# Performance work log

Measured on AMD Instinct MI355X. Metric: run time of the kernel, lower is better.

Reference implementation:

```python
import jax, jax.numpy as jnp
import numpy as np

EPS = 1e-4
B, D, DOUT = 8192, 4096, 4096


def setup_inputs() -> dict:
    key = jax.random.key(0)
    k1, k2, k3 = jax.random.split(key, 3)
    x = jax.random.normal(k1, (B, D), dtype=jnp.float32)
    # Linear layer params (torch nn.Linear: y = x @ W.T + b)
    W = jax.random.normal(k2, (DOUT, D), dtype=jnp.float32) * (1.0 / np.sqrt(D))
    b = jax.random.normal(k3, (DOUT,), dtype=jnp.float32) * 0.01
    return {"x": x, "W": W, "b": b}


def reference(x, W, b):
    # hess = sum_b x[b] outer x[b] + eps*I  == X^T X + eps*I (a GEMM, not a
    # materialized [B,D,D] broadcast like the torch source)
    d = x.shape[1]
    hess = jnp.einsum('bi,bj->ij', x, x) + EPS * jnp.eye(d, dtype=x.dtype)
    out = x @ W.T + b  # wrapped nn.Linear
    return out, hess
```

## Files before the change

kernel.cpp:

```cpp
#include <hip/hip_runtime.h>
#include <hip/hip_bf16.h>

#define BDIM 8192
#define DDIM 4096
#define DOUTD 4096

typedef __attribute__((ext_vector_type(8))) short short8;
typedef __attribute__((ext_vector_type(16))) float floatx16;

__device__ inline unsigned short f32_to_bf16_rne(float f) {
    unsigned int u = __float_as_uint(f);
    unsigned int lsb = (u >> 16) & 1u;
    u += 0x7fffu + lsb;
    return (unsigned short)(u >> 16);
}

__device__ inline void gload_lds16(const void* g, void* lds) {
    __builtin_amdgcn_global_load_lds(
        (const __attribute__((address_space(1))) void*)g,
        (__attribute__((address_space(3))) void*)lds,
        16, 0, 0);
}

__global__ __launch_bounds__(256)
void convert_transpose_x(const float* __restrict__ x,
                         unsigned short* __restrict__ xb,
                         unsigned short* __restrict__ xT) {
    __shared__ __align__(16) unsigned short tile[64][72];
    const int t = threadIdx.x;
    const int tb = blockIdx.x * 64;
    const int td = blockIdx.y * 64;
#pragma unroll
    for (int p = 0; p < 4; ++p) {
        int c = t + p * 256;
        int row  = c >> 4;
        int col4 = (c & 15) << 2;
        float4 v = *(const float4*)&x[(size_t)(tb + row) * DDIM + td + col4];
        ushort4 o;
        o.x = f32_to_bf16_rne(v.x);
        o.y = f32_to_bf16_rne(v.y);
        o.z = f32_to_bf16_rne(v.z);
        o.w = f32_to_bf16_rne(v.w);
        *(ushort4*)&xb[(size_t)(tb + row) * DDIM + td + col4] = o;
        tile[col4 + 0][row] = o.x;
        tile[col4 + 1][row] = o.y;
        tile[col4 + 2][row] = o.z;
        tile[col4 + 3][row] = o.w;
    }
    __syncthreads();
#pragma unroll
    for (int p = 0; p < 4; ++p) {
        int c = t + p * 256;
        int drow = c >> 4;
        int b4   = (c & 15) << 2;
        ushort4 o = *(const ushort4*)&tile[drow][b4];
        *(ushort4*)&xT[(size_t)(td + drow) * BDIM + tb + b4] = o;
    }
}

__global__ __launch_bounds__(256)
void convert_w_kernel(const float* __restrict__ W, unsigned short* __restrict__ Wb) {
    size_t i = ((size_t)blockIdx.x * 256 + threadIdx.x) * 4;
    float4 v = *(const float4*)&W[i];
    ushort4 o;
    o.x = f32_to_bf16_rne(v.x);
    o.y = f32_to_bf16_rne(v.y);
    o.z = f32_to_bf16_rne(v.z);
    o.w = f32_to_bf16_rne(v.w);
    *(ushort4*)&Wb[i] = o;
}

#define CFENCE() asm volatile("" ::: "memory")
#define BAR() do { CFENCE(); __builtin_amdgcn_s_barrier(); CFENCE(); } while (0)
#define MFMA_BF16 __builtin_amdgcn_mfma_f32_32x32x16_bf16

template <bool HESS>
__global__ __launch_bounds__(512, 2)
void gemm256(const unsigned short* __restrict__ A,
             const unsigned short* __restrict__ B,
             const float* __restrict__ bias,
             float* __restrict__ C,
             int M, int N, int K) {
    __shared__ __align__(16) unsigned short As[32768];
    __shared__ __align__(16) unsigned short Bs[32768];

    const int t    = threadIdx.x;
    const int lane = t & 63;
    const int w    = t >> 6;
    const int lm   = lane & 31;
    const int hi   = lane >> 5;
    const int key2 = (lm >> 2) & 3;
    const int wm   = w >> 2;
    const int wn   = w & 3;
    const size_t bm = (size_t)blockIdx.y * 256;
    const size_t bn = (size_t)blockIdx.x * 256;
    const int NT = K >> 6;

    const int kh_w = w >> 2;
    const int wq   = w & 3;
    const int rsub = lane >> 2;
    const int csrc = (lane & 3) ^ ((lane >> 4) & 3);
    const unsigned short* gA0 = A + (bm + wq * 32 + rsub) * (size_t)K + kh_w * 32 + csrc * 8;
    const unsigned short* gB0 = B + (bn + wq * 32 + rsub) * (size_t)K + kh_w * 32 + csrc * 8;
    char* ldsA = (char*)As + kh_w * 16384 + wq * 2048;
    char* ldsB = (char*)Bs + kh_w * 16384 + wq * 2048;
    const size_t rowK16 = (size_t)16 * K;
    const size_t halfK  = (size_t)128 * K;

#define STAGE_A(tj, h, buf) do {                                   \
        const size_t _ko = (size_t)(tj) * 64 + (size_t)(h) * halfK;\
        char* _d = ldsA + (buf) * 32768 + (h) * 8192;              \
        gload_lds16(gA0 + _ko, _d);                                \
        gload_lds16(gA0 + _ko + rowK16, _d + 1024);                \
    } while (0)
#define STAGE_B(tj, h, buf) do {                                   \
        const size_t _ko = (size_t)(tj) * 64 + (size_t)(h) * halfK;\
        char* _d = ldsB + (buf) * 32768 + (h) * 8192;              \
        gload_lds16(gB0 + _ko, _d);                                \
        gload_lds16(gB0 + _ko + rowK16, _d + 1024);                \
    } while (0)

    const int AROWb = (wm * 128 + lm) * 32;
    const int BROWb = (wn * 32 + lm) * 32;
    int pofs[4];
#pragma unroll
    for (int s = 0; s < 4; ++s)
        pofs[s] = (s >> 1) * 8192 + ((((s & 1) * 2 + hi) ^ key2) * 8);

    floatx16 acc[4][2];
#pragma unroll
    for (int i = 0; i < 4; ++i)
#pragma unroll
        for (int j = 0; j < 2; ++j)
#pragma unroll
            for (int g = 0; g < 16; ++g)
                acc[i][j][g] = 0.f;

    short8 af0[2][4], af1[2][4], bf[4];

    STAGE_B(0, 0, 0);
    STAGE_A(0, 0, 0);
    STAGE_A(0, 1, 0);
    STAGE_B(0, 1, 0);
    STAGE_B(1, 0, 1);
    STAGE_A(1, 0, 1);
    STAGE_A(1, 1, 1);
    asm volatile("s_waitcnt vmcnt(6)" ::: "memory");
    BAR();

    for (int j = 0; j < NT; ++j) {
        const int cur = j & 1;
        const int ab  = cur * 16384;

#pragma unroll
        for (int mi = 0; mi < 2; ++mi)
#pragma unroll
            for (int s = 0; s < 4; ++s)
                af0[mi][s] = *(const short8*)&As[ab + AROWb + mi * 1024 + pofs[s]];
#pragma unroll
        for (int s = 0; s < 4; ++s)
            bf[s] = *(const short8*)&Bs[ab + BROWb + pofs[s]];
        if (j + 1 < NT) STAGE_B(j + 1, 1, cur ^ 1);
        BAR();
        __builtin_amdgcn_s_setprio(1);
#pragma unroll
        for (int s = 0; s < 4; ++s) {
            acc[0][0] = MFMA_BF16(af0[0][s], bf[s], acc[0][0], 0, 0, 0);
            acc[1][0] = MFMA_BF16(af0[1][s], bf[s], acc[1][0], 0, 0, 0);
        }
        __builtin_amdgcn_s_setprio(0);
        asm volatile("s_waitcnt lgkmcnt(0)" ::: "memory");
        BAR();

#pragma unroll
        for (int mi = 0; mi < 2; ++mi)
#pragma unroll
            for (int s = 0; s < 4; ++s)
                af1[mi][s] = *(const short8*)&As[ab + AROWb + 2048 + mi * 1024 + pofs[s]];
        if (j + 2 < NT) STAGE_B(j + 2, 0, cur);
        BAR();
        __builtin_amdgcn_s_setprio(1);
#pragma unroll
        for (int s = 0; s < 4; ++s) {
            acc[2][0] = MFMA_BF16(af1[0][s], bf[s], acc[2][0], 0, 0, 0);
            acc[3][0] = MFMA_BF16(af1[1][s], bf[s], acc[3][0], 0, 0, 0);
        }
        __builtin_amdgcn_s_setprio(0);
        asm volatile("s_waitcnt lgkmcnt(0)" ::: "memory");
        BAR();

#pragma unroll
        for (int s = 0; s < 4; ++s)
            bf[s] = *(const short8*)&Bs[ab + BROWb + 4096 + pofs[s]];
        if (j + 2 < NT) STAGE_A(j + 2, 0, cur);
        BAR();
        __builtin_amdgcn_s_setprio(1);
#pragma unroll
        for (int s = 0; s < 4; ++s) {
            acc[2][1] = MFMA_BF16(af1[0][s], bf[s], acc[2][1], 0, 0, 0);
            acc[3][1] = MFMA_BF16(af1[1][s], bf[s], acc[3][1], 0, 0, 0);
        }
        __builtin_amdgcn_s_setprio(0);
        asm volatile("s_waitcnt lgkmcnt(0)" ::: "memory");
        BAR();

        if (j + 2 < NT) STAGE_A(j + 2, 1, cur);
        BAR();
        __builtin_amdgcn_s_setprio(1);
#pragma unroll
        for (int s = 0; s < 4; ++s) {
            acc[0][1] = MFMA_BF16(af0[0][s], bf[s], acc[0][1], 0, 0, 0);
            acc[1][1] = MFMA_BF16(af0[1][s], bf[s], acc[1][1], 0, 0, 0);
        }
        __builtin_amdgcn_s_setprio(0);
        if (j < NT - 2)       asm volatile("s_waitcnt vmcnt(6)" ::: "memory");
        else if (j == NT - 2) asm volatile("s_waitcnt vmcnt(0)" ::: "memory");
        BAR();
    }
#undef STAGE_A
#undef STAGE_B

    float bv[2];
#pragma unroll
    for (int n2 = 0; n2 < 2; ++n2)
        bv[n2] = HESS ? 0.f : bias[bn + n2 * 128 + wn * 32 + lm];
#pragma unroll
    for (int m4 = 0; m4 < 4; ++m4) {
        const size_t mbase = bm + wm * 128 + (m4 >> 1) * 64 + (m4 & 1) * 32 + 4 * hi;
#pragma unroll
        for (int n2 = 0; n2 < 2; ++n2) {
            const size_t n = bn + n2 * 128 + wn * 32 + lm;
#pragma unroll
            for (int reg = 0; reg < 16; ++reg) {
                const size_t m = mbase + (reg & 3) + 8 * (reg >> 2);
                float v = acc[m4][n2][reg] + bv[n2];
                if (HESS && m == n) v += 1e-4f;
                C[m * N + n] = v;
            }
        }
    }
}

extern "C" void kernel_launch(void* const* d_in, const int* in_sizes, int n_in,
                              void* d_out, int out_size, void* d_ws, size_t ws_size,
                              hipStream_t stream) {
    const float* x = (const float*)d_in[0];
    const float* W = (const float*)d_in[1];
    const float* b = (const float*)d_in[2];

    float* out  = (float*)d_out;
    float* hess = out + (size_t)BDIM * DOUTD;

    unsigned short* xb = (unsigned short*)d_ws;
    unsigned short* xT = xb + (size_t)BDIM * DDIM;
    unsigned short* Wb = xT + (size_t)BDIM * DDIM;

    convert_transpose_x<<<dim3(BDIM / 64, DDIM / 64), 256, 0, stream>>>(x, xb, xT);
    convert_w_kernel<<<((size_t)DOUTD * DDIM) / 1024, 256, 0, stream>>>(W, Wb);

    gemm256<false><<<dim3(DOUTD / 256, BDIM / 256), 512, 0, stream>>>(
        xb, Wb, b, out, BDIM, DOUTD, DDIM);
    gemm256<true><<<dim3(DDIM / 256, DDIM / 256), 512, 0, stream>>>(
        xT, xT, nullptr, hess, DDIM, DDIM, BDIM);
}
```

Measured before the change: 858.7 us.

## Restructure GEMM main loop into k-slice phases with register double-buffered fragments

```diff
diff --git a/kernel.cpp b/kernel.cpp
--- a/kernel.cpp
+++ b/kernel.cpp
@@ -96,36 +96,37 @@
     const size_t bn = (size_t)blockIdx.x * 256;
     const int NT = K >> 6;
 
-    const int kh_w = w >> 2;
-    const int wq   = w & 3;
     const int rsub = lane >> 2;
     const int csrc = (lane & 3) ^ ((lane >> 4) & 3);
-    const unsigned short* gA0 = A + (bm + wq * 32 + rsub) * (size_t)K + kh_w * 32 + csrc * 8;
-    const unsigned short* gB0 = B + (bn + wq * 32 + rsub) * (size_t)K + kh_w * 32 + csrc * 8;
-    char* ldsA = (char*)As + kh_w * 16384 + wq * 2048;
-    char* ldsB = (char*)Bs + kh_w * 16384 + wq * 2048;
+    const unsigned short* gA0 = A + (bm + w * 32 + rsub) * (size_t)K + csrc * 8;
+    const unsigned short* gB0 = B + (bn + w * 32 + rsub) * (size_t)K + csrc * 8;
+    char* ldsA = (char*)As + w * 2048;
+    char* ldsB = (char*)Bs + w * 2048;
     const size_t rowK16 = (size_t)16 * K;
-    const size_t halfK  = (size_t)128 * K;
-
-#define STAGE_A(tj, h, buf) do {                                   \
-        const size_t _ko = (size_t)(tj) * 64 + (size_t)(h) * halfK;\
-        char* _d = ldsA + (buf) * 32768 + (h) * 8192;              \
+
+#define STAGE_A(tj, r, buf) do {                                   \
+        const size_t _ko = (size_t)(tj) * 64 + (size_t)(r) * 32;   \
+        char* _d = ldsA + (buf) * 32768 + (r) * 16384;             \
         gload_lds16(gA0 + _ko, _d);                                \
         gload_lds16(gA0 + _ko + rowK16, _d + 1024);                \
     } while (0)
-#define STAGE_B(tj, h, buf) do {                                   \
-        const size_t _ko = (size_t)(tj) * 64 + (size_t)(h) * halfK;\
-        char* _d = ldsB + (buf) * 32768 + (h) * 8192;              \
+#define STAGE_B(tj, r, buf) do {                                   \
+        const size_t _ko = (size_t)(tj) * 64 + (size_t)(r) * 32;   \
+        char* _d = ldsB + (buf) * 32768 + (r) * 16384;             \
         gload_lds16(gB0 + _ko, _d);                                \
         gload_lds16(gB0 + _ko + rowK16, _d + 1024);                \
     } while (0)
 
-    const int AROWb = (wm * 128 + lm) * 32;
-    const int BROWb = (wn * 32 + lm) * 32;
-    int pofs[4];
+    const int arow0 = (wm * 128 +  0 + lm) * 32;
+    const int arow1 = (wm * 128 + 32 + lm) * 32;
+    const int arow2 = (wm * 128 + 64 + lm) * 32;
+    const int arow3 = (wm * 128 + 96 + lm) * 32;
+    const int brow0 = (  0 + wn * 32 + lm) * 32;
+    const int brow1 = (128 + wn * 32 + lm) * 32;
+    int pos[4];
 #pragma unroll
     for (int s = 0; s < 4; ++s)
-        pofs[s] = (s >> 1) * 8192 + ((((s & 1) * 2 + hi) ^ key2) * 8);
+        pos[s] = (s >> 1) * 8192 + ((((s & 1) * 2 + hi) ^ key2) * 8);
 
     floatx16 acc[4][2];
 #pragma unroll
@@ -136,89 +137,83 @@
             for (int g = 0; g < 16; ++g)
                 acc[i][j][g] = 0.f;
 
-    short8 af0[2][4], af1[2][4], bf[4];
-
-    STAGE_B(0, 0, 0);
-    STAGE_A(0, 0, 0);
-    STAGE_A(0, 1, 0);
-    STAGE_B(0, 1, 0);
-    STAGE_B(1, 0, 1);
-    STAGE_A(1, 0, 1);
-    STAGE_A(1, 1, 1);
+    short8 af[2][4], bf[2][2];
+
+#define READS(tt, bufofs, set) do {                                 \
+        const int _o = (bufofs) + pos[tt];                          \
+        af[set][0] = *(const short8*)&As[_o + arow0];               \
+        af[set][1] = *(const short8*)&As[_o + arow1];               \
+        af[set][2] = *(const short8*)&As[_o + arow2];               \
+        af[set][3] = *(const short8*)&As[_o + arow3];               \
+        bf[set][0] = *(const short8*)&Bs[_o + brow0];               \
+        bf[set][1] = *(const short8*)&Bs[_o + brow1];               \
+    } while (0)
+
+#define MM(set) do {                                                        \
+        acc[0][0] = MFMA_BF16(af[set][0], bf[set][0], acc[0][0], 0, 0, 0);  \
+        acc[1][0] = MFMA_BF16(af[set][1], bf[set][0], acc[1][0], 0, 0, 0);  \
+        acc[2][0] = MFMA_BF16(af[set][2], bf[set][0], acc[2][0], 0, 0, 0);  \
+        acc[3][0] = MFMA_BF16(af[set][3], bf[set][0], acc[3][0], 0, 0, 0);  \
+        acc[0][1] = MFMA_BF16(af[set][0], bf[set][1], acc[0][1], 0, 0, 0);  \
+        acc[1][1] = MFMA_BF16(af[set][1], bf[set][1], acc[1][1], 0, 0, 0);  \
+        acc[2][1] = MFMA_BF16(af[set][2], bf[set][1], acc[2][1], 0, 0, 0);  \
+        acc[3][1] = MFMA_BF16(af[set][3], bf[set][1], acc[3][1], 0, 0, 0);  \
+    } while (0)
+
+    STAGE_B(0, 0, 0); STAGE_A(0, 0, 0); STAGE_B(0, 1, 0); STAGE_A(0, 1, 0);
+    STAGE_B(1, 0, 1); STAGE_A(1, 0, 1); STAGE_B(1, 1, 1);
     asm volatile("s_waitcnt vmcnt(6)" ::: "memory");
     BAR();
+    READS(0, 0, 0);
 
     for (int j = 0; j < NT; ++j) {
-        const int cur = j & 1;
-        const int ab  = cur * 16384;
-
-#pragma unroll
-        for (int mi = 0; mi < 2; ++mi)
-#pragma unroll
-            for (int s = 0; s < 4; ++s)
-                af0[mi][s] = *(const short8*)&As[ab + AROWb + mi * 1024 + pofs[s]];
-#pragma unroll
-        for (int s = 0; s < 4; ++s)
-            bf[s] = *(const short8*)&Bs[ab + BROWb + pofs[s]];
-        if (j + 1 < NT) STAGE_B(j + 1, 1, cur ^ 1);
-        BAR();
-        __builtin_amdgcn_s_setprio(1);
-#pragma unroll
-        for (int s = 0; s < 4; ++s) {
-            acc[0][0] = MFMA_BF16(af0[0][s], bf[s], acc[0][0], 0, 0, 0);
-            acc[1][0] = MFMA_BF16(af0[1][s], bf[s], acc[1][0], 0, 0, 0);
-        }
-        __builtin_amdgcn_s_setprio(0);
-        asm volatile("s_waitcnt lgkmcnt(0)" ::: "memory");
-        BAR();
-
-#pragma unroll
-        for (int mi = 0; mi < 2; ++mi)
-#pragma unroll
-            for (int s = 0; s < 4; ++s)
-                af1[mi][s] = *(const short8*)&As[ab + AROWb + 2048 + mi * 1024 + pofs[s]];
-        if (j + 2 < NT) STAGE_B(j + 2, 0, cur);
-        BAR();
-        __builtin_amdgcn_s_setprio(1);
-#pragma unroll
-        for (int s = 0; s < 4; ++s) {
-            acc[2][0] = MFMA_BF16(af1[0][s], bf[s], acc[2][0], 0, 0, 0);
-            acc[3][0] = MFMA_BF16(af1[1][s], bf[s], acc[3][0], 0, 0, 0);
-        }
-        __builtin_amdgcn_s_setprio(0);
-        asm volatile("s_waitcnt lgkmcnt(0)" ::: "memory");
-        BAR();
-
-#pragma unroll
-        for (int s = 0; s < 4; ++s)
-            bf[s] = *(const short8*)&Bs[ab + BROWb + 4096 + pofs[s]];
-        if (j + 2 < NT) STAGE_A(j + 2, 0, cur);
-        BAR();
-        __builtin_amdgcn_s_setprio(1);
-#pragma unroll
-        for (int s = 0; s < 4; ++s) {
-            acc[2][1] = MFMA_BF16(af1[0][s], bf[s], acc[2][1], 0, 0, 0);
-            acc[3][1] = MFMA_BF16(af1[1][s], bf[s], acc[3][1], 0, 0, 0);
-        }
-        __builtin_amdgcn_s_setprio(0);
-        asm volatile("s_waitcnt lgkmcnt(0)" ::: "memory");
-        BAR();
-
-        if (j + 2 < NT) STAGE_A(j + 2, 1, cur);
-        BAR();
-        __builtin_amdgcn_s_setprio(1);
-#pragma unroll
-        for (int s = 0; s < 4; ++s) {
-            acc[0][1] = MFMA_BF16(af0[0][s], bf[s], acc[0][1], 0, 0, 0);
-            acc[1][1] = MFMA_BF16(af0[1][s], bf[s], acc[1][1], 0, 0, 0);
-        }
-        __builtin_amdgcn_s_setprio(0);
-        if (j < NT - 2)       asm volatile("s_waitcnt vmcnt(6)" ::: "memory");
-        else if (j == NT - 2) asm volatile("s_waitcnt vmcnt(0)" ::: "memory");
-        BAR();
-    }
+        const int b   = j & 1;
+        const int ab  = b * 16384;
+        const int ab2 = (b ^ 1) * 16384;
+        const int j1 = (j + 1 < NT) ? j + 1 : NT - 1;
+        const int j2 = (j + 2 < NT) ? j + 2 : NT - 1;
+
+        READS(1, ab, 1);
+        STAGE_A(j1, 1, b ^ 1);
+        BAR();
+        __builtin_amdgcn_s_setprio(1);
+        MM(0);
+        __builtin_amdgcn_s_setprio(0);
+        asm volatile("s_waitcnt vmcnt(8) lgkmcnt(0)" ::: "memory");
+        __builtin_amdgcn_sched_barrier(0);
+        BAR();
+
+        READS(2, ab, 0);
+        STAGE_B(j2, 0, b);
+        BAR();
+        __builtin_amdgcn_s_setprio(1);
+        MM(1);
+        __builtin_amdgcn_s_setprio(0);
+        BAR();
+
+        READS(3, ab, 1);
+        STAGE_A(j2, 0, b);
+        BAR();
+        __builtin_amdgcn_s_setprio(1);
+        MM(0);
+        __builtin_amdgcn_s_setprio(0);
+        asm volatile("s_waitcnt vmcnt(8) lgkmcnt(0)" ::: "memory");
+        __builtin_amdgcn_sched_barrier(0);
+        BAR();
+
+        READS(0, ab2, 0);
+        STAGE_B(j2, 1, b);
+        BAR();
+        __builtin_amdgcn_s_setprio(1);
+        MM(1);
+        __builtin_amdgcn_s_setprio(0);
+        BAR();
+    }
+    asm volatile("s_waitcnt vmcnt(0)" ::: "memory");
 #undef STAGE_A
 #undef STAGE_B
+#undef READS
+#undef MM
 
     float bv[2];
 #pragma unroll
@@ -226,7 +221,7 @@
         bv[n2] = HESS ? 0.f : bias[bn + n2 * 128 + wn * 32 + lm];
 #pragma unroll
     for (int m4 = 0; m4 < 4; ++m4) {
-        const size_t mbase = bm + wm * 128 + (m4 >> 1) * 64 + (m4 & 1) * 32 + 4 * hi;
+        const size_t mbase = bm + wm * 128 + m4 * 32 + 4 * hi;
 #pragma unroll
         for (int n2 = 0; n2 < 2; ++n2) {
             const size_t n = bn + n2 * 128 + wn * 32 + lm;
```

Result: slower. 935.2 us (+8.9%).

## Unroll GEMM main loop by two and prefetch next tile's LDS fragments early

Applied to the files above, without the earlier changes.

```diff
diff --git a/kernel.cpp b/kernel.cpp
--- a/kernel.cpp
+++ b/kernel.cpp
@@ -122,10 +122,10 @@
 
     const int AROWb = (wm * 128 + lm) * 32;
     const int BROWb = (wn * 32 + lm) * 32;
-    int pofs[4];
+    int pos[4];
 #pragma unroll
     for (int s = 0; s < 4; ++s)
-        pofs[s] = (s >> 1) * 8192 + ((((s & 1) * 2 + hi) ^ key2) * 8);
+        pos[s] = (s >> 1) * 8192 + ((((s & 1) * 2 + hi) ^ key2) * 8);
 
     floatx16 acc[4][2];
 #pragma unroll
@@ -138,87 +138,96 @@
 
     short8 af0[2][4], af1[2][4], bf[4];
 
-    STAGE_B(0, 0, 0);
-    STAGE_A(0, 0, 0);
-    STAGE_A(0, 1, 0);
-    STAGE_B(0, 1, 0);
-    STAGE_B(1, 0, 1);
-    STAGE_A(1, 0, 1);
-    STAGE_A(1, 1, 1);
+#define READS_EARLY(AB2) do {                                              \
+        _Pragma("unroll")                                                  \
+        for (int s = 0; s < 4; ++s)                                        \
+            af0[0][s] = *(const short8*)&As[(AB2) + AROWb + pos[s]];       \
+        bf[0] = *(const short8*)&Bs[(AB2) + BROWb + pos[0]];               \
+        bf[1] = *(const short8*)&Bs[(AB2) + BROWb + pos[1]];               \
+    } while (0)
+
+#define TILE_BODY(J, BUFC) do {                                            \
+        constexpr int AB  = (BUFC) * 16384;                                \
+        constexpr int AB2 = ((BUFC) ^ 1) * 16384;                          \
+               \
+        _Pragma("unroll")                                                  \
+        for (int s = 0; s < 4; ++s)                                        \
+            af0[1][s] = *(const short8*)&As[AB + AROWb + 1024 + pos[s]];   \
+        bf[2] = *(const short8*)&Bs[AB + BROWb + pos[2]];                  \
+        bf[3] = *(const short8*)&Bs[AB + BROWb + pos[3]];                  \
+        if ((J) + 1 < NT) STAGE_B((J) + 1, 1, (BUFC) ^ 1);                 \
+        BAR();                                                             \
+        __builtin_amdgcn_s_setprio(1);                                     \
+        _Pragma("unroll")                                                  \
+        for (int s = 0; s < 4; ++s) {                                      \
+            acc[0][0] = MFMA_BF16(af0[0][s], bf[s], acc[0][0], 0, 0, 0);   \
+            acc[1][0] = MFMA_BF16(af0[1][s], bf[s], acc[1][0], 0, 0, 0);   \
+        }                                                                  \
+        __builtin_amdgcn_s_setprio(0);                                     \
+        asm volatile("s_waitcnt lgkmcnt(0)" ::: "memory");                 \
+        BAR();                                                             \
+                              \
+        _Pragma("unroll")                                                  \
+        for (int mi = 0; mi < 2; ++mi)                                     \
+            _Pragma("unroll")                                              \
+            for (int s = 0; s < 4; ++s)                                    \
+                af1[mi][s] = *(const short8*)&As[AB + AROWb + 2048 + mi * 1024 + pos[s]]; \
+        if ((J) + 2 < NT) STAGE_B((J) + 2, 0, (BUFC));                     \
+        BAR();                                                             \
+        __builtin_amdgcn_s_setprio(1);                                     \
+        _Pragma("unroll")                                                  \
+        for (int s = 0; s < 4; ++s) {                                      \
+            acc[2][0] = MFMA_BF16(af1[0][s], bf[s], acc[2][0], 0, 0, 0);   \
+            acc[3][0] = MFMA_BF16(af1[1][s], bf[s], acc[3][0], 0, 0, 0);   \
+        }                                                                  \
+        __builtin_amdgcn_s_setprio(0);                                     \
+        asm volatile("s_waitcnt lgkmcnt(0)" ::: "memory");                 \
+        BAR();                                                             \
+                           \
+        _Pragma("unroll")                                                  \
+        for (int s = 0; s < 4; ++s)                                        \
+            bf[s] = *(const short8*)&Bs[AB + BROWb + 4096 + pos[s]];       \
+        if ((J) + 2 < NT) STAGE_A((J) + 2, 0, (BUFC));                     \
+        BAR();                                                             \
+        __builtin_amdgcn_s_setprio(1);                                     \
+        _Pragma("unroll")                                                  \
+        for (int s = 0; s < 4; ++s) {                                      \
+            acc[2][1] = MFMA_BF16(af1[0][s], bf[s], acc[2][1], 0, 0, 0);   \
+            acc[3][1] = MFMA_BF16(af1[1][s], bf[s], acc[3][1], 0, 0, 0);   \
+        }                                                                  \
+        __builtin_amdgcn_s_setprio(0);                                     \
+        asm volatile("s_waitcnt lgkmcnt(0)" ::: "memory");                 \
+        BAR();                                                             \
+        \
+        if ((J) + 2 < NT) STAGE_A((J) + 2, 1, (BUFC));                     \
+        if ((J) < NT - 2)       asm volatile("s_waitcnt vmcnt(6)" ::: "memory"); \
+        else if ((J) == NT - 2) asm volatile("s_waitcnt vmcnt(0)" ::: "memory"); \
+        BAR();                                                             \
+        __builtin_amdgcn_s_setprio(1);                                     \
+        _Pragma("unroll")                                                  \
+        for (int s = 0; s < 4; ++s) {                                      \
+            acc[0][1] = MFMA_BF16(af0[0][s], bf[s], acc[0][1], 0, 0, 0);   \
+            acc[1][1] = MFMA_BF16(af0[1][s], bf[s], acc[1][1], 0, 0, 0);   \
+        }                                                                  \
+        __builtin_amdgcn_s_setprio(0);                                     \
+        if ((J) + 1 < NT) READS_EARLY(AB2);                                \
+        BAR();                                                             \
+    } while (0)
+
+    STAGE_B(0, 0, 0); STAGE_A(0, 0, 0); STAGE_B(0, 1, 0); STAGE_A(0, 1, 0);
+    STAGE_B(1, 0, 1); STAGE_A(1, 0, 1); STAGE_A(1, 1, 1);
     asm volatile("s_waitcnt vmcnt(6)" ::: "memory");
     BAR();
-
-    for (int j = 0; j < NT; ++j) {
-        const int cur = j & 1;
-        const int ab  = cur * 16384;
-
-#pragma unroll
-        for (int mi = 0; mi < 2; ++mi)
-#pragma unroll
-            for (int s = 0; s < 4; ++s)
-                af0[mi][s] = *(const short8*)&As[ab + AROWb + mi * 1024 + pofs[s]];
-#pragma unroll
-        for (int s = 0; s < 4; ++s)
-            bf[s] = *(const short8*)&Bs[ab + BROWb + pofs[s]];
-        if (j + 1 < NT) STAGE_B(j + 1, 1, cur ^ 1);
-        BAR();
-        __builtin_amdgcn_s_setprio(1);
-#pragma unroll
-        for (int s = 0; s < 4; ++s) {
-            acc[0][0] = MFMA_BF16(af0[0][s], bf[s], acc[0][0], 0, 0, 0);
-            acc[1][0] = MFMA_BF16(af0[1][s], bf[s], acc[1][0], 0, 0, 0);
-        }
-        __builtin_amdgcn_s_setprio(0);
-        asm volatile("s_waitcnt lgkmcnt(0)" ::: "memory");
-        BAR();
-
-#pragma unroll
-        for (int mi = 0; mi < 2; ++mi)
-#pragma unroll
-            for (int s = 0; s < 4; ++s)
-                af1[mi][s] = *(const short8*)&As[ab + AROWb + 2048 + mi * 1024 + pofs[s]];
-        if (j + 2 < NT) STAGE_B(j + 2, 0, cur);
-        BAR();
-        __builtin_amdgcn_s_setprio(1);
-#pragma unroll
-        for (int s = 0; s < 4; ++s) {
-            acc[2][0] = MFMA_BF16(af1[0][s], bf[s], acc[2][0], 0, 0, 0);
-            acc[3][0] = MFMA_BF16(af1[1][s], bf[s], acc[3][0], 0, 0, 0);
-        }
-        __builtin_amdgcn_s_setprio(0);
-        asm volatile("s_waitcnt lgkmcnt(0)" ::: "memory");
-        BAR();
-
-#pragma unroll
-        for (int s = 0; s < 4; ++s)
-            bf[s] = *(const short8*)&Bs[ab + BROWb + 4096 + pofs[s]];
-        if (j + 2 < NT) STAGE_A(j + 2, 0, cur);
-        BAR();
-        __builtin_amdgcn_s_setprio(1);
-#pragma unroll
-        for (int s = 0; s < 4; ++s) {
-            acc[2][1] = MFMA_BF16(af1[0][s], bf[s], acc[2][1], 0, 0, 0);
-            acc[3][1] = MFMA_BF16(af1[1][s], bf[s], acc[3][1], 0, 0, 0);
-        }
-        __builtin_amdgcn_s_setprio(0);
-        asm volatile("s_waitcnt lgkmcnt(0)" ::: "memory");
-        BAR();
-
-        if (j + 2 < NT) STAGE_A(j + 2, 1, cur);
-        BAR();
-        __builtin_amdgcn_s_setprio(1);
-#pragma unroll
-        for (int s = 0; s < 4; ++s) {
-            acc[0][1] = MFMA_BF16(af0[0][s], bf[s], acc[0][1], 0, 0, 0);
-            acc[1][1] = MFMA_BF16(af0[1][s], bf[s], acc[1][1], 0, 0, 0);
-        }
-        __builtin_amdgcn_s_setprio(0);
-        if (j < NT - 2)       asm volatile("s_waitcnt vmcnt(6)" ::: "memory");
-        else if (j == NT - 2) asm volatile("s_waitcnt vmcnt(0)" ::: "memory");
-        BAR();
+    READS_EARLY(0);
+
+    for (int jj = 0; jj < NT; jj += 2) {
+        TILE_BODY(jj, 0);
+        TILE_BODY(jj + 1, 1);
     }
 #undef STAGE_A
 #undef STAGE_B
+#undef READS_EARLY
+#undef TILE_BODY
 
     float bv[2];
 #pragma unroll
@@ -226,7 +235,7 @@
         bv[n2] = HESS ? 0.f : bias[bn + n2 * 128 + wn * 32 + lm];
 #pragma unroll
     for (int m4 = 0; m4 < 4; ++m4) {
-        const size_t mbase = bm + wm * 128 + (m4 >> 1) * 64 + (m4 & 1) * 32 + 4 * hi;
+        const size_t mbase = bm + wm * 128 + m4 * 32 + 4 * hi;
 #pragma unroll
         for (int n2 = 0; n2 < 2; ++n2) {
             const size_t n = bn + n2 * 128 + wn * 32 + lm;
```

New measurement: 863.1 us. Within noise of the previous version (+0.5%).
